# Kernel optimization log

Hardware: AMD Instinct MI355X
Metric: run time of the kernel (lower is better)

Reference implementation:

```python
import jax, jax.numpy as jnp
import numpy as np

B = 4096
N_QUBITS = 4
N_LAYERS = 3
C64 = jnp.complex64


def setup_inputs() -> dict:
    key = jax.random.key(0)
    ks = jax.random.split(key, 14)
    f = jax.random.normal
    return {
        "x": f(ks[0], (B, 1, 28, 28), jnp.float32),
        "qparams": f(ks[1], (N_LAYERS, N_QUBITS, 3), jnp.float32),
        "dw4_w": f(ks[2], (4, 1, 4, 4), jnp.float32) * 0.1,
        "dw4_b": f(ks[3], (4,), jnp.float32) * 0.1,
        "pw4_w": f(ks[4], (4, 4, 1, 1), jnp.float32) * 0.3,
        "pw4_b": f(ks[5], (4,), jnp.float32) * 0.1,
        "dw8_w": f(ks[6], (4, 1, 8, 8), jnp.float32) * 0.05,
        "dw8_b": f(ks[7], (4,), jnp.float32) * 0.1,
        "pw8_w": f(ks[8], (4, 4, 1, 1), jnp.float32) * 0.3,
        "pw8_b": f(ks[9], (4,), jnp.float32) * 0.1,
        "res_w": f(ks[10], (4, 1, 1, 1), jnp.float32) * 0.3,
        "res_b": f(ks[11], (4,), jnp.float32) * 0.1,
        "head_w": f(ks[12], (10, 4 * 3 * 14 * 14), jnp.float32) * 0.02,
        "head_b": f(ks[13], (10,), jnp.float32) * 0.02,
    }


def _rx(t):
    c = jnp.cos(t / 2).astype(C64)
    s = (-1j * jnp.sin(t / 2)).astype(C64)
    return jnp.stack([jnp.stack([c, s]), jnp.stack([s, c])])


def _ry(t):
    c = jnp.cos(t / 2)
    s = jnp.sin(t / 2)
    return jnp.stack([jnp.stack([c, -s]), jnp.stack([s, c])]).astype(C64)


def _rz(t):
    z = jnp.zeros((), C64)
    return jnp.stack([jnp.stack([jnp.exp(-0.5j * t).astype(C64), z]),
                      jnp.stack([z, jnp.exp(0.5j * t).astype(C64)])])


def _apply_1q(state, U, wire):
    # state: (n,2,2,2,2); U: (2,2) shared across patches
    st = jnp.moveaxis(state, wire + 1, -1)
    st = jnp.einsum('ij,n...j->n...i', U, st)
    return jnp.moveaxis(st, -1, wire + 1)


def _apply_1q_batched(state, U, wire):
    # U: (n,2,2), one gate per patch (input encoding)
    st = jnp.moveaxis(state, wire + 1, -1)
    st = jnp.einsum('nij,n...j->n...i', U, st)
    return jnp.moveaxis(st, -1, wire + 1)


def _cnot(state, c, t):
    a, b = jnp.split(state, 2, axis=c + 1)
    return jnp.concatenate([a, jnp.flip(b, axis=t + 1)], axis=c + 1)


def _quantum_features(patches, params):
    # patches: (n,4) angles; returns (n,4) PauliZ expectations
    n = patches.shape[0]
    state = jnp.zeros((n, 16), C64).at[:, 0].set(1.0).reshape(n, 2, 2, 2, 2)
    c = jnp.cos(patches / 2)
    s = jnp.sin(patches / 2)
    for q in range(N_QUBITS):
        Uq = jnp.stack([jnp.stack([c[:, q], -s[:, q]], -1),
                        jnp.stack([s[:, q], c[:, q]], -1)], -2).astype(C64)
        state = _apply_1q_batched(state, Uq, q)
    for l in range(N_LAYERS):
        for q in range(N_QUBITS):
            state = _apply_1q(state, _rx(params[l, q, 0]), q)
            state = _apply_1q(state, _ry(params[l, q, 1]), q)
            state = _apply_1q(state, _rz(params[l, q, 2]), q)
        for q in range(N_QUBITS - 1):
            state = _cnot(state, q, q + 1)
        state = _cnot(state, N_QUBITS - 1, 0)
    probs = jnp.real(state * jnp.conj(state))  # (n,2,2,2,2)
    ez = [jnp.sum(jnp.take(probs, 0, axis=q + 1) - jnp.take(probs, 1, axis=q + 1),
                  axis=(1, 2, 3)) for q in range(N_QUBITS)]
    return jnp.stack(ez, -1).astype(jnp.float32)


def _conv(x, w, b, stride):
    y = jax.lax.conv_general_dilated(x, w, (stride, stride), 'VALID',
                                     dimension_numbers=('NCHW', 'OIHW', 'NCHW'))
    return y + b[None, :, None, None]


def _forward(x, qparams, dw4_w, dw4_b, pw4_w, pw4_b, dw8_w, dw8_b, pw8_w, pw8_b,
             res_w, res_b, head_w, head_b):
    b = x.shape[0]
    # residual branch: 1x1 conv then 2x2 avg-pool down to the 14x14 grid
    res = _conv(x, res_w, res_b, 1)                      # (B,4,28,28)
    res = res.reshape(b, 4, 14, 2, 14, 2).mean(axis=(3, 5))  # (B,4,14,14)
    # quantum branch over non-overlapping 2x2 patches
    patches = x[:, 0].reshape(b, 14, 2, 14, 2).transpose(0, 1, 3, 2, 4)
    patches = patches.reshape(b * 14 * 14, 4)
    feat2 = _quantum_features(patches, qparams).reshape(b, 14, 14, 4)
    # multi-scale conv branches, upsampled (nearest) to the 14x14 grid
    feat4 = jax.nn.relu(_conv(_conv(x, dw4_w, dw4_b, 4), pw4_w, pw4_b, 1))  # (B,4,7,7)
    feat4 = jnp.repeat(jnp.repeat(feat4, 2, axis=2), 2, axis=3)             # (B,4,14,14)
    feat8 = jax.nn.relu(_conv(_conv(x, dw8_w, dw8_b, 8), pw8_w, pw8_b, 1))  # (B,4,3,3)
    feat8 = jax.image.resize(feat8, (b, 4, 14, 14), 'nearest')
    f4 = jnp.transpose(feat4, (0, 2, 3, 1))
    f8 = jnp.transpose(feat8, (0, 2, 3, 1))
    r = jnp.transpose(res, (0, 2, 3, 1))
    out = jnp.concatenate([feat2, f4, f8], axis=3) + jnp.tile(r, (1, 1, 1, 3))
    logits = out.reshape(b, -1) @ head_w.T + head_b
    return jax.nn.log_softmax(logits, axis=-1)


def reference(x, qparams, dw4_w, dw4_b, pw4_w, pw4_b, dw8_w, dw8_b, pw8_w, pw8_b,
              res_w, res_b, head_w, head_b):
    return _forward(x, qparams, dw4_w, dw4_b, pw4_w, pw4_b, dw8_w, dw8_b,
                    pw8_w, pw8_b, res_w, res_b, head_w, head_b)
```

## Files before the change

### kernel.cpp

```cpp
#include <hip/hip_runtime.h>

#define WS_T    0
#define WS_HQ   512
#define WS_WA   8352
#define WS_H4   10312
#define WS_H8   12272
#define WS_C10  12632

__device__ __forceinline__ float4 f4fma(const float4 a, const float s, const float4 c) {
  return {fmaf(a.x, s, c.x), fmaf(a.y, s, c.y), fmaf(a.z, s, c.z), fmaf(a.w, s, c.w)};
}
__device__ __forceinline__ float4 f4fma4(const float4 a, const float4 b, const float4 c) {
  return {fmaf(a.x, b.x, c.x), fmaf(a.y, b.y, c.y), fmaf(a.z, b.z, c.z), fmaf(a.w, b.w, c.w)};
}
__device__ __forceinline__ float hsum4(const float4 a) {
  return a.x + a.y + a.z + a.w;
}

__global__ __launch_bounds__(256) void prep_kernel(
    const float* __restrict__ qp, const float* __restrict__ hw,
    const float* __restrict__ res_w, const float* __restrict__ res_b,
    const float* __restrict__ hb, float* __restrict__ ws) {
  __shared__ float row[2352];
  __shared__ float cred[4];
  __shared__ float Sr[16][16];
  __shared__ float Si[16][16];
  __shared__ float csc[36], css[36];
  __shared__ float Afs[256][4];
  const int t = threadIdx.x;

  if (blockIdx.x < 10) {
    const int k = blockIdx.x;
    for (int i = t; i < 2352; i += 256) row[i] = hw[k * 2352 + i];
    __syncthreads();
    float cpart = 0.f;
    if (t < 196) {
      const int b12 = t * 12;
      float4 h = {row[b12], row[b12 + 1], row[b12 + 2], row[b12 + 3]};
      ((float4*)(ws + WS_HQ))[k * 196 + t] = h;
      float wa = 0.f;
#pragma unroll
      for (int c = 0; c < 4; ++c) {
        const float s3 = row[b12 + c] + row[b12 + 4 + c] + row[b12 + 8 + c];
        wa += res_w[c] * s3;
        cpart += res_b[c] * s3;
      }
      ws[WS_WA + k * 196 + t] = wa;
    }
    if (t < 49) {
      const int i4 = t / 7, j4 = t % 7;
      float4 s = {0.f, 0.f, 0.f, 0.f};
#pragma unroll
      for (int di = 0; di < 2; ++di)
#pragma unroll
        for (int dj = 0; dj < 2; ++dj) {
          const int pos = (2 * i4 + di) * 14 + 2 * j4 + dj;
          s.x += row[pos * 12 + 4]; s.y += row[pos * 12 + 5];
          s.z += row[pos * 12 + 6]; s.w += row[pos * 12 + 7];
        }
      ((float4*)(ws + WS_H4))[k * 49 + t] = s;
    }
    if (t < 9) {
      const int i8 = t / 3, j8 = t % 3;
      const int pi0 = (i8 == 0) ? 0 : ((i8 == 1) ? 5 : 9);
      const int pi1 = (i8 == 0) ? 5 : ((i8 == 1) ? 9 : 14);
      const int pj0 = (j8 == 0) ? 0 : ((j8 == 1) ? 5 : 9);
      const int pj1 = (j8 == 0) ? 5 : ((j8 == 1) ? 9 : 14);
      float4 s = {0.f, 0.f, 0.f, 0.f};
      for (int pi = pi0; pi < pi1; ++pi)
        for (int pj = pj0; pj < pj1; ++pj) {
          const int pos = pi * 14 + pj;
          s.x += row[pos * 12 + 8]; s.y += row[pos * 12 + 9];
          s.z += row[pos * 12 + 10]; s.w += row[pos * 12 + 11];
        }
      ((float4*)(ws + WS_H8))[k * 9 + t] = s;
    }
#pragma unroll
    for (int off = 32; off > 0; off >>= 1) cpart += __shfl_xor(cpart, off);
    if ((t & 63) == 0) cred[t >> 6] = cpart;
    __syncthreads();
    if (t == 0) ws[WS_C10 + k] = hb[k] + cred[0] + cred[1] + cred[2] + cred[3];
    return;
  }

  if (t < 36) {
    float th = 0.5f * qp[t];
    csc[t] = cosf(th);
    css[t] = sinf(th);
  }
  Sr[t >> 4][t & 15] = ((t >> 4) == (t & 15)) ? 1.f : 0.f;
  Si[t >> 4][t & 15] = 0.f;
  __syncthreads();

  const int col = t >> 3, pp = t & 7;
  for (int l = 0; l < 3; ++l) {
    for (int q = 0; q < 4; ++q) {
      const int m = 8 >> q;
      for (int r = 0; r < 3; ++r) {
        if (t < 128) {
          const float c = csc[l * 12 + q * 3 + r];
          const float s = css[l * 12 + q * 3 + r];
          const int k = ((pp & ~(m - 1)) << 1) | (pp & (m - 1));
          const int k1 = k | m;
          float a0r = Sr[col][k],  a0i = Si[col][k];
          float a1r = Sr[col][k1], a1i = Si[col][k1];
          float n0r, n0i, n1r, n1i;
          if (r == 0) {
            n0r = c * a0r + s * a1i;  n0i = c * a0i - s * a1r;
            n1r = c * a1r + s * a0i;  n1i = c * a1i - s * a0r;
          } else if (r == 1) {
            n0r = c * a0r - s * a1r;  n0i = c * a0i - s * a1i;
            n1r = s * a0r + c * a1r;  n1i = s * a0i + c * a1i;
          } else {
            n0r = c * a0r + s * a0i;  n0i = c * a0i - s * a0r;
            n1r = c * a1r - s * a1i;  n1i = c * a1i + s * a1r;
          }
          Sr[col][k] = n0r;  Si[col][k] = n0i;
          Sr[col][k1] = n1r; Si[col][k1] = n1i;
        }
        __syncthreads();
      }
    }
    for (int e = 0; e < 4; ++e) {
      if (t < 64) {
        const int c2 = t >> 2, p2 = t & 3;
        const int mc = 8 >> e;
        const int mt = 8 >> ((e + 1) & 3);
        const int rest = 15 & ~(mc | mt);
        const int rl = rest & (-rest);
        const int rh = rest ^ rl;
        const int k = mc | ((p2 & 1) ? rl : 0) | ((p2 & 2) ? rh : 0);
        const int k1 = k | mt;
        float tr = Sr[c2][k]; Sr[c2][k] = Sr[c2][k1]; Sr[c2][k1] = tr;
        float ti = Si[c2][k]; Si[c2][k] = Si[c2][k1]; Si[c2][k1] = ti;
      }
      __syncthreads();
    }
  }

  {
    const int i = t >> 4, j = t & 15;
    float a0 = 0.f, a1 = 0.f, a2 = 0.f, a3 = 0.f;
    for (int k = 0; k < 16; ++k) {
      float pr = Sr[i][k] * Sr[j][k] + Si[i][k] * Si[j][k];
      a0 += (k & 8) ? -pr : pr;
      a1 += (k & 4) ? -pr : pr;
      a2 += (k & 2) ? -pr : pr;
      a3 += (k & 1) ? -pr : pr;
    }
    Afs[t][0] = a0; Afs[t][1] = a1; Afs[t][2] = a2; Afs[t][3] = a3;
  }
  __syncthreads();

  for (int o = t; o < 324; o += 256) {
    const int mi = o >> 2, q = o & 3;
    const int m0 = mi / 27, m1 = (mi / 9) % 3, m2 = (mi / 3) % 3, m3 = mi % 3;
    const int mm[4] = {m0, m1, m2, m3};
    float acc = 0.f;
    for (int c = 0; c < 16; ++c) {
      int ii = 0, jj = 0; float sg = 1.f;
      for (int qb = 0; qb < 4; ++qb) {
        const int cb = (c >> qb) & 1, bit = 8 >> qb, mq = mm[qb];
        if (mq == 2) { if (cb) ii |= bit; else jj |= bit; }
        else if (cb) { ii |= bit; jj |= bit; if (mq == 1) sg = -sg; }
      }
      acc += sg * Afs[ii * 16 + jj][q];
    }
    ws[WS_T + mi * 4 + q] = acc * 0.0625f;
  }
}

__global__ __launch_bounds__(256, 4) void qmain_kernel(
    const float* __restrict__ x, const float4* __restrict__ T4,
    const float4* __restrict__ HQ4, const float* __restrict__ WA,
    const float4* __restrict__ H44, const float4* __restrict__ H84,
    const float* __restrict__ C10,
    const float* __restrict__ dw4_w, const float* __restrict__ dw4_b,
    const float* __restrict__ pw4_w, const float* __restrict__ pw4_b,
    const float* __restrict__ dw8_w, const float* __restrict__ dw8_b,
    const float* __restrict__ pw8_w, const float* __restrict__ pw8_b,
    float* __restrict__ out, const int B) {
  __shared__ __align__(16) float xs[4 * 792];
  const int t = threadIdx.x;
  const int w = t >> 6, lane = t & 63;
  const int img = blockIdx.x * 4 + w;
  float* xw = xs + w * 792;
  const float4* xw4 = (const float4*)xw;

  if (img < B) {
    const float4* xg = (const float4*)(x + img * 784);
#pragma unroll
    for (int it = 0; it < 4; ++it) {
      const int idx = it * 64 + lane;
      if (idx < 196) ((float4*)xw)[idx] = xg[idx];
    }
  }
  __syncthreads();

  if (img >= B) return;

  float acc[10];
#pragma unroll
  for (int k = 0; k < 10; ++k) acc[k] = 0.f;

#pragma unroll 1
  for (int r = 0; r < 4; ++r) {
    const int p = r * 64 + lane;
    if (p < 196) {
      const int pi = p / 14, pj = p % 14;
      const int base = 56 * pi + 2 * pj;
      const float2 a01 = *(const float2*)(xw + base);
      const float2 a23 = *(const float2*)(xw + base + 28);
      const float a0 = a01.x, a1 = a01.y, a2 = a23.x, a3 = a23.y;
      float c0, s0, c1, s1, c2, s2, c3, s3;
      __sincosf(a0, &s0, &c0);
      __sincosf(a1, &s1, &c1);
      __sincosf(a2, &s2, &c2);
      __sincosf(a3, &s3, &c3);
      const float w01[9] = {1.f, c1, s1, c0, c0 * c1, c0 * s1, s0, s0 * c1, s0 * s1};
      float4 e = {0.f, 0.f, 0.f, 0.f};
#pragma unroll
      for (int g = 0; g < 9; ++g) {
        const float4 t0 = T4[g * 9 + 0], t1 = T4[g * 9 + 1], t2 = T4[g * 9 + 2];
        const float4 t3 = T4[g * 9 + 3], t4 = T4[g * 9 + 4], t5 = T4[g * 9 + 5];
        const float4 t6 = T4[g * 9 + 6], t7 = T4[g * 9 + 7], t8 = T4[g * 9 + 8];
        const float4 u0 = f4fma(t2, s3, f4fma(t1, c3, t0));
        const float4 u1 = f4fma(t5, s3, f4fma(t4, c3, t3));
        const float4 u2 = f4fma(t8, s3, f4fma(t7, c3, t6));
        const float4 inner = f4fma(u2, s2, f4fma(u1, c2, u0));
        e = f4fma(inner, w01[g], e);
      }
      const float avg = 0.25f * (a0 + a1 + a2 + a3);
#pragma unroll
      for (int k = 0; k < 10; ++k) {
        const float4 h = HQ4[k * 196 + p];
        acc[k] += fmaf(h.x, e.x, fmaf(h.y, e.y,
                  fmaf(h.z, e.z, fmaf(h.w, e.w, WA[k * 196 + p] * avg))));
      }
    } else {
      const int u = p - 196;
      if (u < 49) {
        const int i = u / 7, j = u % 7;
        const float4* w44 = (const float4*)dw4_w;
        float4 q0 = {0.f, 0.f, 0.f, 0.f}, q1 = q0, q2 = q0, q3 = q0;
#pragma unroll
        for (int uu = 0; uu < 4; ++uu) {
          const float4 xa = xw4[(4 * i + uu) * 7 + j];
          q0 = f4fma4(w44[0 + uu], xa, q0);
          q1 = f4fma4(w44[4 + uu], xa, q1);
          q2 = f4fma4(w44[8 + uu], xa, q2);
          q3 = f4fma4(w44[12 + uu], xa, q3);
        }
        const float y0 = hsum4(q0) + dw4_b[0];
        const float y1 = hsum4(q1) + dw4_b[1];
        const float y2 = hsum4(q2) + dw4_b[2];
        const float y3 = hsum4(q3) + dw4_b[3];
        float z[4];
#pragma unroll
        for (int o = 0; o < 4; ++o) {
          float zz = pw4_b[o];
          zz = fmaf(pw4_w[o * 4 + 0], y0, zz);
          zz = fmaf(pw4_w[o * 4 + 1], y1, zz);
          zz = fmaf(pw4_w[o * 4 + 2], y2, zz);
          zz = fmaf(pw4_w[o * 4 + 3], y3, zz);
          z[o] = fmaxf(zz, 0.f);
        }
#pragma unroll
        for (int k = 0; k < 10; ++k) {
          const float4 h = H44[k * 49 + u];
          acc[k] += fmaf(h.x, z[0], fmaf(h.y, z[1], fmaf(h.z, z[2], h.w * z[3])));
        }
      } else if (u < 58) {
        const int pos = u - 49;
        const int i8 = pos / 3, j8 = pos % 3;
        const float4* w84 = (const float4*)dw8_w;
        float4 e0 = {0.f, 0.f, 0.f, 0.f}, e1 = e0, e2 = e0, e3 = e0;
#pragma unroll
        for (int uu = 0; uu < 8; ++uu) {
          const float4 xa = xw4[(8 * i8 + uu) * 7 + 2 * j8];
          const float4 xb = xw4[(8 * i8 + uu) * 7 + 2 * j8 + 1];
          e0 = f4fma4(w84[0 + uu * 2], xa, e0);
          e0 = f4fma4(w84[1 + uu * 2], xb, e0);
          e1 = f4fma4(w84[16 + uu * 2], xa, e1);
          e1 = f4fma4(w84[17 + uu * 2], xb, e1);
          e2 = f4fma4(w84[32 + uu * 2], xa, e2);
          e2 = f4fma4(w84[33 + uu * 2], xb, e2);
          e3 = f4fma4(w84[48 + uu * 2], xa, e3);
          e3 = f4fma4(w84[49 + uu * 2], xb, e3);
        }
        const float d0 = hsum4(e0) + dw8_b[0];
        const float d1 = hsum4(e1) + dw8_b[1];
        const float d2 = hsum4(e2) + dw8_b[2];
        const float d3 = hsum4(e3) + dw8_b[3];
        float z[4];
#pragma unroll
        for (int o = 0; o < 4; ++o) {
          float zz = pw8_b[o];
          zz = fmaf(pw8_w[o * 4 + 0], d0, zz);
          zz = fmaf(pw8_w[o * 4 + 1], d1, zz);
          zz = fmaf(pw8_w[o * 4 + 2], d2, zz);
          zz = fmaf(pw8_w[o * 4 + 3], d3, zz);
          z[o] = fmaxf(zz, 0.f);
        }
#pragma unroll
        for (int k = 0; k < 10; ++k) {
          const float4 h = H84[k * 9 + pos];
          acc[k] += fmaf(h.x, z[0], fmaf(h.y, z[1], fmaf(h.z, z[2], h.w * z[3])));
        }
      }
    }
  }

#pragma unroll
  for (int k = 0; k < 10; ++k) {
    float v = acc[k];
    v += __shfl_xor(v, 1);
    v += __shfl_xor(v, 2);
    v += __shfl_xor(v, 4);
    v += __shfl_xor(v, 8);
    v += __shfl_xor(v, 16);
    v += __shfl_xor(v, 32);
    acc[k] = v;
  }

  float lg[10], m = -1e30f;
#pragma unroll
  for (int k = 0; k < 10; ++k) {
    lg[k] = acc[k] + C10[k];
    m = fmaxf(m, lg[k]);
  }
  float se = 0.f;
#pragma unroll
  for (int k = 0; k < 10; ++k) se += __expf(lg[k] - m);
  const float ls = m + __logf(se);
  if (lane < 10) {
    float v = lg[0];
#pragma unroll
    for (int k = 1; k < 10; ++k)
      if (lane == k) v = lg[k];
    out[img * 10 + lane] = v - ls;
  }
}

extern "C" void kernel_launch(void* const* d_in, const int* in_sizes, int n_in,
                              void* d_out, int out_size, void* d_ws, size_t ws_size,
                              hipStream_t stream) {
  const float* x      = (const float*)d_in[0];
  const float* qp     = (const float*)d_in[1];
  const float* dw4_w  = (const float*)d_in[2];
  const float* dw4_b  = (const float*)d_in[3];
  const float* pw4_w  = (const float*)d_in[4];
  const float* pw4_b  = (const float*)d_in[5];
  const float* dw8_w  = (const float*)d_in[6];
  const float* dw8_b  = (const float*)d_in[7];
  const float* pw8_w  = (const float*)d_in[8];
  const float* pw8_b  = (const float*)d_in[9];
  const float* res_w  = (const float*)d_in[10];
  const float* res_b  = (const float*)d_in[11];
  const float* head_w = (const float*)d_in[12];
  const float* head_b = (const float*)d_in[13];
  float* out = (float*)d_out;
  float* ws = (float*)d_ws;
  const int B = in_sizes[0] / 784;

  hipLaunchKernelGGL(prep_kernel, dim3(11), dim3(256), 0, stream,
                     qp, head_w, res_w, res_b, head_b, ws);
  hipLaunchKernelGGL(qmain_kernel, dim3((B + 3) / 4), dim3(256), 0, stream,
                     x, (const float4*)(ws + WS_T),
                     (const float4*)(ws + WS_HQ), ws + WS_WA,
                     (const float4*)(ws + WS_H4), (const float4*)(ws + WS_H8),
                     ws + WS_C10,
                     dw4_w, dw4_b, pw4_w, pw4_b, dw8_w, dw8_b, pw8_w, pw8_b,
                     out, B);
}
```

Before: 33.86 us.

## Split each image across two wavefronts and run prep quantum sim in one wave

The main kernel now assigns two wavefronts per image instead of one. Each wave processes half of the 196 quantum patches, one wave handles the 4x4 conv branch and the other the 8x8 branch, and the partial logits are combined through shared memory before log-softmax. The launch grid doubles and the occupancy hint is raised to 8. The prep kernel's state simulation now runs in a single 64-thread wavefront, which removes the many block-wide barriers. The cost is an extra LDS reduction and barrier in the main kernel, plus more blocks to schedule.

After: 76.70 us. 127% more time.

```diff
diff --git a/kernel.cpp b/kernel.cpp
--- a/kernel.cpp
+++ b/kernel.cpp
@@ -83,23 +83,30 @@
     return;
   }
 
+  if (t >= 64) return;
+
   if (t < 36) {
     float th = 0.5f * qp[t];
     csc[t] = cosf(th);
     css[t] = sinf(th);
   }
-  Sr[t >> 4][t & 15] = ((t >> 4) == (t & 15)) ? 1.f : 0.f;
-  Si[t >> 4][t & 15] = 0.f;
-  __syncthreads();
-
-  const int col = t >> 3, pp = t & 7;
+#pragma unroll
+  for (int h = 0; h < 4; ++h) {
+    const int idx = t + 64 * h;
+    Sr[idx >> 4][idx & 15] = ((idx >> 4) == (idx & 15)) ? 1.f : 0.f;
+    Si[idx >> 4][idx & 15] = 0.f;
+  }
+
   for (int l = 0; l < 3; ++l) {
     for (int q = 0; q < 4; ++q) {
       const int m = 8 >> q;
       for (int r = 0; r < 3; ++r) {
-        if (t < 128) {
-          const float c = csc[l * 12 + q * 3 + r];
-          const float s = css[l * 12 + q * 3 + r];
+        const float c = csc[l * 12 + q * 3 + r];
+        const float s = css[l * 12 + q * 3 + r];
+#pragma unroll
+        for (int h = 0; h < 2; ++h) {
+          const int idx = t + 64 * h;
+          const int col = idx >> 3, pp = idx & 7;
           const int k = ((pp & ~(m - 1)) << 1) | (pp & (m - 1));
           const int k1 = k | m;
           float a0r = Sr[col][k],  a0i = Si[col][k];
@@ -118,28 +125,26 @@
           Sr[col][k] = n0r;  Si[col][k] = n0i;
           Sr[col][k1] = n1r; Si[col][k1] = n1i;
         }
-        __syncthreads();
       }
     }
     for (int e = 0; e < 4; ++e) {
-      if (t < 64) {
-        const int c2 = t >> 2, p2 = t & 3;
-        const int mc = 8 >> e;
-        const int mt = 8 >> ((e + 1) & 3);
-        const int rest = 15 & ~(mc | mt);
-        const int rl = rest & (-rest);
-        const int rh = rest ^ rl;
-        const int k = mc | ((p2 & 1) ? rl : 0) | ((p2 & 2) ? rh : 0);
-        const int k1 = k | mt;
-        float tr = Sr[c2][k]; Sr[c2][k] = Sr[c2][k1]; Sr[c2][k1] = tr;
-        float ti = Si[c2][k]; Si[c2][k] = Si[c2][k1]; Si[c2][k1] = ti;
-      }
-      __syncthreads();
-    }
-  }
-
-  {
-    const int i = t >> 4, j = t & 15;
+      const int c2 = t >> 2, p2 = t & 3;
+      const int mc = 8 >> e;
+      const int mt = 8 >> ((e + 1) & 3);
+      const int rest = 15 & ~(mc | mt);
+      const int rl = rest & (-rest);
+      const int rh = rest ^ rl;
+      const int k = mc | ((p2 & 1) ? rl : 0) | ((p2 & 2) ? rh : 0);
+      const int k1 = k | mt;
+      float tr = Sr[c2][k]; Sr[c2][k] = Sr[c2][k1]; Sr[c2][k1] = tr;
+      float ti = Si[c2][k]; Si[c2][k] = Si[c2][k1]; Si[c2][k1] = ti;
+    }
+  }
+
+#pragma unroll
+  for (int h = 0; h < 4; ++h) {
+    const int o = t + 64 * h;
+    const int i = o >> 4, j = o & 15;
     float a0 = 0.f, a1 = 0.f, a2 = 0.f, a3 = 0.f;
     for (int k = 0; k < 16; ++k) {
       float pr = Sr[i][k] * Sr[j][k] + Si[i][k] * Si[j][k];
@@ -148,29 +153,32 @@
       a2 += (k & 2) ? -pr : pr;
       a3 += (k & 1) ? -pr : pr;
     }
-    Afs[t][0] = a0; Afs[t][1] = a1; Afs[t][2] = a2; Afs[t][3] = a3;
-  }
-  __syncthreads();
-
-  for (int o = t; o < 324; o += 256) {
-    const int mi = o >> 2, q = o & 3;
-    const int m0 = mi / 27, m1 = (mi / 9) % 3, m2 = (mi / 3) % 3, m3 = mi % 3;
-    const int mm[4] = {m0, m1, m2, m3};
-    float acc = 0.f;
-    for (int c = 0; c < 16; ++c) {
-      int ii = 0, jj = 0; float sg = 1.f;
-      for (int qb = 0; qb < 4; ++qb) {
-        const int cb = (c >> qb) & 1, bit = 8 >> qb, mq = mm[qb];
-        if (mq == 2) { if (cb) ii |= bit; else jj |= bit; }
-        else if (cb) { ii |= bit; jj |= bit; if (mq == 1) sg = -sg; }
-      }
-      acc += sg * Afs[ii * 16 + jj][q];
-    }
-    ws[WS_T + mi * 4 + q] = acc * 0.0625f;
-  }
-}
-
-__global__ __launch_bounds__(256, 4) void qmain_kernel(
+    Afs[o][0] = a0; Afs[o][1] = a1; Afs[o][2] = a2; Afs[o][3] = a3;
+  }
+
+#pragma unroll
+  for (int h = 0; h < 6; ++h) {
+    const int o = t + 64 * h;
+    if (o < 324) {
+      const int mi = o >> 2, q = o & 3;
+      const int m0 = mi / 27, m1 = (mi / 9) % 3, m2 = (mi / 3) % 3, m3 = mi % 3;
+      const int mm[4] = {m0, m1, m2, m3};
+      float acc = 0.f;
+      for (int c = 0; c < 16; ++c) {
+        int ii = 0, jj = 0; float sg = 1.f;
+        for (int qb = 0; qb < 4; ++qb) {
+          const int cb = (c >> qb) & 1, bit = 8 >> qb, mq = mm[qb];
+          if (mq == 2) { if (cb) ii |= bit; else jj |= bit; }
+          else if (cb) { ii |= bit; jj |= bit; if (mq == 1) sg = -sg; }
+        }
+        acc += sg * Afs[ii * 16 + jj][q];
+      }
+      ws[WS_T + mi * 4 + q] = acc * 0.0625f;
+    }
+  }
+}
+
+__global__ __launch_bounds__(256, 8) void qmain_kernel(
     const float* __restrict__ x, const float4* __restrict__ T4,
     const float4* __restrict__ HQ4, const float* __restrict__ WA,
     const float4* __restrict__ H44, const float4* __restrict__ H84,
@@ -180,66 +188,74 @@
     const float* __restrict__ dw8_w, const float* __restrict__ dw8_b,
     const float* __restrict__ pw8_w, const float* __restrict__ pw8_b,
     float* __restrict__ out, const int B) {
-  __shared__ __align__(16) float xs[4 * 792];
+  __shared__ __align__(16) float xs[2 * 792];
+  __shared__ float accw[4][10];
   const int t = threadIdx.x;
   const int w = t >> 6, lane = t & 63;
-  const int img = blockIdx.x * 4 + w;
-  float* xw = xs + w * 792;
+  const int il = w >> 1, pw = w & 1;
+  const int img = blockIdx.x * 2 + il;
+  float* xw = xs + il * 792;
   const float4* xw4 = (const float4*)xw;
-
-  if (img < B) {
+  const bool ok = (img < B);
+
+  if (ok) {
     const float4* xg = (const float4*)(x + img * 784);
-#pragma unroll
-    for (int it = 0; it < 4; ++it) {
-      const int idx = it * 64 + lane;
-      if (idx < 196) ((float4*)xw)[idx] = xg[idx];
+    const int i0 = pw * 98 + lane;
+    ((float4*)xw)[i0] = xg[i0];
+    if (lane < 34) {
+      const int i1 = pw * 98 + 64 + lane;
+      ((float4*)xw)[i1] = xg[i1];
+    }
+  }
+
+  float acc[10];
+#pragma unroll
+  for (int k = 0; k < 10; ++k) acc[k] = 0.f;
+
+  if (ok) {
+#pragma unroll 1
+    for (int r = 0; r < 2; ++r) {
+      const int p = pw * 98 + r * 64 + lane;
+      if (r == 0 || lane < 34) {
+        const int pi = p / 14, pj = p % 14;
+        const int base = 56 * pi + 2 * pj;
+        const float2 a01 = *(const float2*)(xw + base);
+        const float2 a23 = *(const float2*)(xw + base + 28);
+        const float a0 = a01.x, a1 = a01.y, a2 = a23.x, a3 = a23.y;
+        float c0, s0, c1, s1, c2, s2, c3, s3;
+        __sincosf(a0, &s0, &c0);
+        __sincosf(a1, &s1, &c1);
+        __sincosf(a2, &s2, &c2);
+        __sincosf(a3, &s3, &c3);
+        const float w01[9] = {1.f, c1, s1, c0, c0 * c1, c0 * s1, s0, s0 * c1, s0 * s1};
+        float4 e = {0.f, 0.f, 0.f, 0.f};
+#pragma unroll
+        for (int g = 0; g < 9; ++g) {
+          const float4 t0 = T4[g * 9 + 0], t1 = T4[g * 9 + 1], t2 = T4[g * 9 + 2];
+          const float4 t3 = T4[g * 9 + 3], t4 = T4[g * 9 + 4], t5 = T4[g * 9 + 5];
+          const float4 t6 = T4[g * 9 + 6], t7 = T4[g * 9 + 7], t8 = T4[g * 9 + 8];
+          const float4 u0 = f4fma(t2, s3, f4fma(t1, c3, t0));
+          const float4 u1 = f4fma(t5, s3, f4fma(t4, c3, t3));
+          const float4 u2 = f4fma(t8, s3, f4fma(t7, c3, t6));
+          const float4 inner = f4fma(u2, s2, f4fma(u1, c2, u0));
+          e = f4fma(inner, w01[g], e);
+        }
+        const float avg = 0.25f * (a0 + a1 + a2 + a3);
+#pragma unroll
+        for (int k = 0; k < 10; ++k) {
+          const float4 h = HQ4[k * 196 + p];
+          acc[k] += fmaf(h.x, e.x, fmaf(h.y, e.y,
+                    fmaf(h.z, e.z, fmaf(h.w, e.w, WA[k * 196 + p] * avg))));
+        }
+      }
     }
   }
   __syncthreads();
 
-  if (img >= B) return;
-
-  float acc[10];
-#pragma unroll
-  for (int k = 0; k < 10; ++k) acc[k] = 0.f;
-
-#pragma unroll 1
-  for (int r = 0; r < 4; ++r) {
-    const int p = r * 64 + lane;
-    if (p < 196) {
-      const int pi = p / 14, pj = p % 14;
-      const int base = 56 * pi + 2 * pj;
-      const float2 a01 = *(const float2*)(xw + base);
-      const float2 a23 = *(const float2*)(xw + base + 28);
-      const float a0 = a01.x, a1 = a01.y, a2 = a23.x, a3 = a23.y;
-      float c0, s0, c1, s1, c2, s2, c3, s3;
-      __sincosf(a0, &s0, &c0);
-      __sincosf(a1, &s1, &c1);
-      __sincosf(a2, &s2, &c2);
-      __sincosf(a3, &s3, &c3);
-      const float w01[9] = {1.f, c1, s1, c0, c0 * c1, c0 * s1, s0, s0 * c1, s0 * s1};
-      float4 e = {0.f, 0.f, 0.f, 0.f};
-#pragma unroll
-      for (int g = 0; g < 9; ++g) {
-        const float4 t0 = T4[g * 9 + 0], t1 = T4[g * 9 + 1], t2 = T4[g * 9 + 2];
-        const float4 t3 = T4[g * 9 + 3], t4 = T4[g * 9 + 4], t5 = T4[g * 9 + 5];
-        const float4 t6 = T4[g * 9 + 6], t7 = T4[g * 9 + 7], t8 = T4[g * 9 + 8];
-        const float4 u0 = f4fma(t2, s3, f4fma(t1, c3, t0));
-        const float4 u1 = f4fma(t5, s3, f4fma(t4, c3, t3));
-        const float4 u2 = f4fma(t8, s3, f4fma(t7, c3, t6));
-        const float4 inner = f4fma(u2, s2, f4fma(u1, c2, u0));
-        e = f4fma(inner, w01[g], e);
-      }
-      const float avg = 0.25f * (a0 + a1 + a2 + a3);
-#pragma unroll
-      for (int k = 0; k < 10; ++k) {
-        const float4 h = HQ4[k * 196 + p];
-        acc[k] += fmaf(h.x, e.x, fmaf(h.y, e.y,
-                  fmaf(h.z, e.z, fmaf(h.w, e.w, WA[k * 196 + p] * avg))));
-      }
-    } else {
-      const int u = p - 196;
-      if (u < 49) {
+  if (ok) {
+    if (pw == 0) {
+      if (lane < 49) {
+        const int u = lane;
         const int i = u / 7, j = u % 7;
         const float4* w44 = (const float4*)dw4_w;
         float4 q0 = {0.f, 0.f, 0.f, 0.f}, q1 = q0, q2 = q0, q3 = q0;
@@ -270,8 +286,10 @@
           const float4 h = H44[k * 49 + u];
           acc[k] += fmaf(h.x, z[0], fmaf(h.y, z[1], fmaf(h.z, z[2], h.w * z[3])));
         }
-      } else if (u < 58) {
-        const int pos = u - 49;
+      }
+    } else {
+      if (lane < 9) {
+        const int pos = lane;
         const int i8 = pos / 3, j8 = pos % 3;
         const float4* w84 = (const float4*)dw8_w;
         float4 e0 = {0.f, 0.f, 0.f, 0.f}, e1 = e0, e2 = e0, e3 = e0;
@@ -322,23 +340,29 @@
     v += __shfl_xor(v, 32);
     acc[k] = v;
   }
-
-  float lg[10], m = -1e30f;
-#pragma unroll
-  for (int k = 0; k < 10; ++k) {
-    lg[k] = acc[k] + C10[k];
-    m = fmaxf(m, lg[k]);
-  }
-  float se = 0.f;
-#pragma unroll
-  for (int k = 0; k < 10; ++k) se += __expf(lg[k] - m);
-  const float ls = m + __logf(se);
-  if (lane < 10) {
-    float v = lg[0];
+  {
+    float v = acc[0];
 #pragma unroll
     for (int k = 1; k < 10; ++k)
-      if (lane == k) v = lg[k];
-    out[img * 10 + lane] = v - ls;
+      if (lane == k) v = acc[k];
+    if (lane < 10) accw[w][lane] = v;
+  }
+  __syncthreads();
+
+  if (pw == 0 && ok) {
+    float lg = -1e30f;
+    if (lane < 10) lg = accw[w][lane] + accw[w + 1][lane] + C10[lane];
+    float mx = lg;
+    mx = fmaxf(mx, __shfl_xor(mx, 1));
+    mx = fmaxf(mx, __shfl_xor(mx, 2));
+    mx = fmaxf(mx, __shfl_xor(mx, 4));
+    mx = fmaxf(mx, __shfl_xor(mx, 8));
+    float ex = (lane < 10) ? __expf(lg - mx) : 0.f;
+    ex += __shfl_xor(ex, 1);
+    ex += __shfl_xor(ex, 2);
+    ex += __shfl_xor(ex, 4);
+    ex += __shfl_xor(ex, 8);
+    if (lane < 10) out[img * 10 + lane] = lg - mx - __logf(ex);
   }
 }
 
@@ -365,7 +389,7 @@
 
   hipLaunchKernelGGL(prep_kernel, dim3(11), dim3(256), 0, stream,
                      qp, head_w, res_w, res_b, head_b, ws);
-  hipLaunchKernelGGL(qmain_kernel, dim3((B + 3) / 4), dim3(256), 0, stream,
+  hipLaunchKernelGGL(qmain_kernel, dim3((B + 1) / 2), dim3(256), 0, stream,
                      x, (const float4*)(ws + WS_T),
                      (const float4*)(ws + WS_HQ), ws + WS_WA,
                      (const float4*)(ws + WS_H4), (const float4*)(ws + WS_H8),
```

## Remove block barriers and give each lane four quantum patches

Applied to the files above, without the earlier changes.

The prep kernel now runs its state-vector simulation on a single 64-lane wavefront and drops every __syncthreads. It relies on in-order shared-memory access within one wavefront instead of block barriers. The main kernel drops the post-load block barrier, since each wavefront only reads the image slice it loaded itself. It also remaps work so lanes 0-48 each handle four quantum patches plus one 4x4 conv output, and lanes 49-57 handle the 8x8 conv, which shares each T4 coefficient load across four patches and removes the divergent four-pass loop. The catch is that correctness now depends on implicit wave-synchronous behaviour, and lanes 58-63 sit idle.

Result: no change. 33.89 us (+0.1%).

```diff
diff --git a/kernel.cpp b/kernel.cpp
--- a/kernel.cpp
+++ b/kernel.cpp
@@ -83,23 +83,30 @@
     return;
   }
 
+  if (t >= 64) return;
+
   if (t < 36) {
     float th = 0.5f * qp[t];
     csc[t] = cosf(th);
     css[t] = sinf(th);
   }
-  Sr[t >> 4][t & 15] = ((t >> 4) == (t & 15)) ? 1.f : 0.f;
-  Si[t >> 4][t & 15] = 0.f;
-  __syncthreads();
-
-  const int col = t >> 3, pp = t & 7;
+#pragma unroll
+  for (int h = 0; h < 4; ++h) {
+    const int idx = t + 64 * h;
+    Sr[idx >> 4][idx & 15] = ((idx >> 4) == (idx & 15)) ? 1.f : 0.f;
+    Si[idx >> 4][idx & 15] = 0.f;
+  }
+
   for (int l = 0; l < 3; ++l) {
     for (int q = 0; q < 4; ++q) {
       const int m = 8 >> q;
       for (int r = 0; r < 3; ++r) {
-        if (t < 128) {
-          const float c = csc[l * 12 + q * 3 + r];
-          const float s = css[l * 12 + q * 3 + r];
+        const float c = csc[l * 12 + q * 3 + r];
+        const float s = css[l * 12 + q * 3 + r];
+#pragma unroll
+        for (int h = 0; h < 2; ++h) {
+          const int idx = t + 64 * h;
+          const int col = idx >> 3, pp = idx & 7;
           const int k = ((pp & ~(m - 1)) << 1) | (pp & (m - 1));
           const int k1 = k | m;
           float a0r = Sr[col][k],  a0i = Si[col][k];
@@ -118,28 +125,26 @@
           Sr[col][k] = n0r;  Si[col][k] = n0i;
           Sr[col][k1] = n1r; Si[col][k1] = n1i;
         }
-        __syncthreads();
       }
     }
     for (int e = 0; e < 4; ++e) {
-      if (t < 64) {
-        const int c2 = t >> 2, p2 = t & 3;
-        const int mc = 8 >> e;
-        const int mt = 8 >> ((e + 1) & 3);
-        const int rest = 15 & ~(mc | mt);
-        const int rl = rest & (-rest);
-        const int rh = rest ^ rl;
-        const int k = mc | ((p2 & 1) ? rl : 0) | ((p2 & 2) ? rh : 0);
-        const int k1 = k | mt;
-        float tr = Sr[c2][k]; Sr[c2][k] = Sr[c2][k1]; Sr[c2][k1] = tr;
-        float ti = Si[c2][k]; Si[c2][k] = Si[c2][k1]; Si[c2][k1] = ti;
-      }
-      __syncthreads();
-    }
-  }
-
-  {
-    const int i = t >> 4, j = t & 15;
+      const int c2 = t >> 2, p2 = t & 3;
+      const int mc = 8 >> e;
+      const int mt = 8 >> ((e + 1) & 3);
+      const int rest = 15 & ~(mc | mt);
+      const int rl = rest & (-rest);
+      const int rh = rest ^ rl;
+      const int k = mc | ((p2 & 1) ? rl : 0) | ((p2 & 2) ? rh : 0);
+      const int k1 = k | mt;
+      float tr = Sr[c2][k]; Sr[c2][k] = Sr[c2][k1]; Sr[c2][k1] = tr;
+      float ti = Si[c2][k]; Si[c2][k] = Si[c2][k1]; Si[c2][k1] = ti;
+    }
+  }
+
+#pragma unroll
+  for (int h = 0; h < 4; ++h) {
+    const int o = t + 64 * h;
+    const int i = o >> 4, j = o & 15;
     float a0 = 0.f, a1 = 0.f, a2 = 0.f, a3 = 0.f;
     for (int k = 0; k < 16; ++k) {
       float pr = Sr[i][k] * Sr[j][k] + Si[i][k] * Si[j][k];
@@ -148,25 +153,28 @@
       a2 += (k & 2) ? -pr : pr;
       a3 += (k & 1) ? -pr : pr;
     }
-    Afs[t][0] = a0; Afs[t][1] = a1; Afs[t][2] = a2; Afs[t][3] = a3;
-  }
-  __syncthreads();
-
-  for (int o = t; o < 324; o += 256) {
-    const int mi = o >> 2, q = o & 3;
-    const int m0 = mi / 27, m1 = (mi / 9) % 3, m2 = (mi / 3) % 3, m3 = mi % 3;
-    const int mm[4] = {m0, m1, m2, m3};
-    float acc = 0.f;
-    for (int c = 0; c < 16; ++c) {
-      int ii = 0, jj = 0; float sg = 1.f;
-      for (int qb = 0; qb < 4; ++qb) {
-        const int cb = (c >> qb) & 1, bit = 8 >> qb, mq = mm[qb];
-        if (mq == 2) { if (cb) ii |= bit; else jj |= bit; }
-        else if (cb) { ii |= bit; jj |= bit; if (mq == 1) sg = -sg; }
-      }
-      acc += sg * Afs[ii * 16 + jj][q];
-    }
-    ws[WS_T + mi * 4 + q] = acc * 0.0625f;
+    Afs[o][0] = a0; Afs[o][1] = a1; Afs[o][2] = a2; Afs[o][3] = a3;
+  }
+
+#pragma unroll
+  for (int h = 0; h < 6; ++h) {
+    const int o = t + 64 * h;
+    if (o < 324) {
+      const int mi = o >> 2, q = o & 3;
+      const int m0 = mi / 27, m1 = (mi / 9) % 3, m2 = (mi / 3) % 3, m3 = mi % 3;
+      const int mm[4] = {m0, m1, m2, m3};
+      float acc = 0.f;
+      for (int c = 0; c < 16; ++c) {
+        int ii = 0, jj = 0; float sg = 1.f;
+        for (int qb = 0; qb < 4; ++qb) {
+          const int cb = (c >> qb) & 1, bit = 8 >> qb, mq = mm[qb];
+          if (mq == 2) { if (cb) ii |= bit; else jj |= bit; }
+          else if (cb) { ii |= bit; jj |= bit; if (mq == 1) sg = -sg; }
+        }
+        acc += sg * Afs[ii * 16 + jj][q];
+      }
+      ws[WS_T + mi * 4 + q] = acc * 0.0625f;
+    }
   }
 }
 
@@ -186,8 +194,9 @@
   const int img = blockIdx.x * 4 + w;
   float* xw = xs + w * 792;
   const float4* xw4 = (const float4*)xw;
-
-  if (img < B) {
+  const bool ok = (img < B);
+
+  if (ok) {
     const float4* xg = (const float4*)(x + img * 784);
 #pragma unroll
     for (int it = 0; it < 4; ++it) {
@@ -195,121 +204,132 @@
       if (idx < 196) ((float4*)xw)[idx] = xg[idx];
     }
   }
-  __syncthreads();
-
-  if (img >= B) return;
 
   float acc[10];
 #pragma unroll
   for (int k = 0; k < 10; ++k) acc[k] = 0.f;
 
-#pragma unroll 1
-  for (int r = 0; r < 4; ++r) {
-    const int p = r * 64 + lane;
-    if (p < 196) {
-      const int pi = p / 14, pj = p % 14;
-      const int base = 56 * pi + 2 * pj;
+  if (ok && lane < 49) {
+    float cc[4][4], ss[4][4], av[4];
+#pragma unroll
+    for (int s = 0; s < 4; ++s) {
+      const int p = 49 * s + lane;
+      const int base = 56 * (p / 14) + 2 * (p % 14);
       const float2 a01 = *(const float2*)(xw + base);
       const float2 a23 = *(const float2*)(xw + base + 28);
-      const float a0 = a01.x, a1 = a01.y, a2 = a23.x, a3 = a23.y;
-      float c0, s0, c1, s1, c2, s2, c3, s3;
-      __sincosf(a0, &s0, &c0);
-      __sincosf(a1, &s1, &c1);
-      __sincosf(a2, &s2, &c2);
-      __sincosf(a3, &s3, &c3);
-      const float w01[9] = {1.f, c1, s1, c0, c0 * c1, c0 * s1, s0, s0 * c1, s0 * s1};
-      float4 e = {0.f, 0.f, 0.f, 0.f};
-#pragma unroll
-      for (int g = 0; g < 9; ++g) {
-        const float4 t0 = T4[g * 9 + 0], t1 = T4[g * 9 + 1], t2 = T4[g * 9 + 2];
-        const float4 t3 = T4[g * 9 + 3], t4 = T4[g * 9 + 4], t5 = T4[g * 9 + 5];
-        const float4 t6 = T4[g * 9 + 6], t7 = T4[g * 9 + 7], t8 = T4[g * 9 + 8];
+      __sincosf(a01.x, &ss[s][0], &cc[s][0]);
+      __sincosf(a01.y, &ss[s][1], &cc[s][1]);
+      __sincosf(a23.x, &ss[s][2], &cc[s][2]);
+      __sincosf(a23.y, &ss[s][3], &cc[s][3]);
+      av[s] = 0.25f * (a01.x + a01.y + a23.x + a23.y);
+    }
+    float4 e[4];
+#pragma unroll
+    for (int s = 0; s < 4; ++s) e[s] = {0.f, 0.f, 0.f, 0.f};
+#pragma unroll 1
+    for (int g = 0; g < 9; ++g) {
+      const float4 t0 = T4[g * 9 + 0], t1 = T4[g * 9 + 1], t2 = T4[g * 9 + 2];
+      const float4 t3 = T4[g * 9 + 3], t4 = T4[g * 9 + 4], t5 = T4[g * 9 + 5];
+      const float4 t6 = T4[g * 9 + 6], t7 = T4[g * 9 + 7], t8 = T4[g * 9 + 8];
+      const int m0 = g / 3, m1 = g % 3;
+#pragma unroll
+      for (int s = 0; s < 4; ++s) {
+        const float c3 = cc[s][3], s3 = ss[s][3];
         const float4 u0 = f4fma(t2, s3, f4fma(t1, c3, t0));
         const float4 u1 = f4fma(t5, s3, f4fma(t4, c3, t3));
         const float4 u2 = f4fma(t8, s3, f4fma(t7, c3, t6));
-        const float4 inner = f4fma(u2, s2, f4fma(u1, c2, u0));
-        e = f4fma(inner, w01[g], e);
-      }
-      const float avg = 0.25f * (a0 + a1 + a2 + a3);
+        const float4 inner = f4fma(u2, ss[s][2], f4fma(u1, cc[s][2], u0));
+        const float f0 = (m0 == 0) ? 1.f : ((m0 == 1) ? cc[s][0] : ss[s][0]);
+        const float f1 = (m1 == 0) ? 1.f : ((m1 == 1) ? cc[s][1] : ss[s][1]);
+        const float wf = (m0 == 0) ? f1 : ((m1 == 0) ? f0 : f0 * f1);
+        e[s] = f4fma(inner, wf, e[s]);
+      }
+    }
+#pragma unroll
+    for (int k = 0; k < 10; ++k) {
+      float a = 0.f;
+#pragma unroll
+      for (int s = 0; s < 4; ++s) {
+        const int p = 49 * s + lane;
+        const float4 h = HQ4[k * 196 + p];
+        a += fmaf(h.x, e[s].x, fmaf(h.y, e[s].y,
+             fmaf(h.z, e[s].z, fmaf(h.w, e[s].w, WA[k * 196 + p] * av[s]))));
+      }
+      acc[k] = a;
+    }
+    {
+      const int u = lane;
+      const int i = u / 7, j = u % 7;
+      const float4* w44 = (const float4*)dw4_w;
+      float4 q0 = {0.f, 0.f, 0.f, 0.f}, q1 = q0, q2 = q0, q3 = q0;
+#pragma unroll
+      for (int uu = 0; uu < 4; ++uu) {
+        const float4 xa = xw4[(4 * i + uu) * 7 + j];
+        q0 = f4fma4(w44[0 + uu], xa, q0);
+        q1 = f4fma4(w44[4 + uu], xa, q1);
+        q2 = f4fma4(w44[8 + uu], xa, q2);
+        q3 = f4fma4(w44[12 + uu], xa, q3);
+      }
+      const float y0 = hsum4(q0) + dw4_b[0];
+      const float y1 = hsum4(q1) + dw4_b[1];
+      const float y2 = hsum4(q2) + dw4_b[2];
+      const float y3 = hsum4(q3) + dw4_b[3];
+      float z[4];
+#pragma unroll
+      for (int o = 0; o < 4; ++o) {
+        float zz = pw4_b[o];
+        zz = fmaf(pw4_w[o * 4 + 0], y0, zz);
+        zz = fmaf(pw4_w[o * 4 + 1], y1, zz);
+        zz = fmaf(pw4_w[o * 4 + 2], y2, zz);
+        zz = fmaf(pw4_w[o * 4 + 3], y3, zz);
+        z[o] = fmaxf(zz, 0.f);
+      }
 #pragma unroll
       for (int k = 0; k < 10; ++k) {
-        const float4 h = HQ4[k * 196 + p];
-        acc[k] += fmaf(h.x, e.x, fmaf(h.y, e.y,
-                  fmaf(h.z, e.z, fmaf(h.w, e.w, WA[k * 196 + p] * avg))));
-      }
-    } else {
-      const int u = p - 196;
-      if (u < 49) {
-        const int i = u / 7, j = u % 7;
-        const float4* w44 = (const float4*)dw4_w;
-        float4 q0 = {0.f, 0.f, 0.f, 0.f}, q1 = q0, q2 = q0, q3 = q0;
-#pragma unroll
-        for (int uu = 0; uu < 4; ++uu) {
-          const float4 xa = xw4[(4 * i + uu) * 7 + j];
-          q0 = f4fma4(w44[0 + uu], xa, q0);
-          q1 = f4fma4(w44[4 + uu], xa, q1);
-          q2 = f4fma4(w44[8 + uu], xa, q2);
-          q3 = f4fma4(w44[12 + uu], xa, q3);
-        }
-        const float y0 = hsum4(q0) + dw4_b[0];
-        const float y1 = hsum4(q1) + dw4_b[1];
-        const float y2 = hsum4(q2) + dw4_b[2];
-        const float y3 = hsum4(q3) + dw4_b[3];
-        float z[4];
-#pragma unroll
-        for (int o = 0; o < 4; ++o) {
-          float zz = pw4_b[o];
-          zz = fmaf(pw4_w[o * 4 + 0], y0, zz);
-          zz = fmaf(pw4_w[o * 4 + 1], y1, zz);
-          zz = fmaf(pw4_w[o * 4 + 2], y2, zz);
-          zz = fmaf(pw4_w[o * 4 + 3], y3, zz);
-          z[o] = fmaxf(zz, 0.f);
-        }
-#pragma unroll
-        for (int k = 0; k < 10; ++k) {
-          const float4 h = H44[k * 49 + u];
-          acc[k] += fmaf(h.x, z[0], fmaf(h.y, z[1], fmaf(h.z, z[2], h.w * z[3])));
-        }
-      } else if (u < 58) {
-        const int pos = u - 49;
-        const int i8 = pos / 3, j8 = pos % 3;
-        const float4* w84 = (const float4*)dw8_w;
-        float4 e0 = {0.f, 0.f, 0.f, 0.f}, e1 = e0, e2 = e0, e3 = e0;
-#pragma unroll
-        for (int uu = 0; uu < 8; ++uu) {
-          const float4 xa = xw4[(8 * i8 + uu) * 7 + 2 * j8];
-          const float4 xb = xw4[(8 * i8 + uu) * 7 + 2 * j8 + 1];
-          e0 = f4fma4(w84[0 + uu * 2], xa, e0);
-          e0 = f4fma4(w84[1 + uu * 2], xb, e0);
-          e1 = f4fma4(w84[16 + uu * 2], xa, e1);
-          e1 = f4fma4(w84[17 + uu * 2], xb, e1);
-          e2 = f4fma4(w84[32 + uu * 2], xa, e2);
-          e2 = f4fma4(w84[33 + uu * 2], xb, e2);
-          e3 = f4fma4(w84[48 + uu * 2], xa, e3);
-          e3 = f4fma4(w84[49 + uu * 2], xb, e3);
-        }
-        const float d0 = hsum4(e0) + dw8_b[0];
-        const float d1 = hsum4(e1) + dw8_b[1];
-        const float d2 = hsum4(e2) + dw8_b[2];
-        const float d3 = hsum4(e3) + dw8_b[3];
-        float z[4];
-#pragma unroll
-        for (int o = 0; o < 4; ++o) {
-          float zz = pw8_b[o];
-          zz = fmaf(pw8_w[o * 4 + 0], d0, zz);
-          zz = fmaf(pw8_w[o * 4 + 1], d1, zz);
-          zz = fmaf(pw8_w[o * 4 + 2], d2, zz);
-          zz = fmaf(pw8_w[o * 4 + 3], d3, zz);
-          z[o] = fmaxf(zz, 0.f);
-        }
-#pragma unroll
-        for (int k = 0; k < 10; ++k) {
-          const float4 h = H84[k * 9 + pos];
-          acc[k] += fmaf(h.x, z[0], fmaf(h.y, z[1], fmaf(h.z, z[2], h.w * z[3])));
-        }
-      }
-    }
-  }
+        const float4 h = H44[k * 49 + u];
+        acc[k] += fmaf(h.x, z[0], fmaf(h.y, z[1], fmaf(h.z, z[2], h.w * z[3])));
+      }
+    }
+  } else if (ok && lane >= 49 && lane < 58) {
+    const int pos = lane - 49;
+    const int i8 = pos / 3, j8 = pos % 3;
+    const float4* w84 = (const float4*)dw8_w;
+    float4 e0 = {0.f, 0.f, 0.f, 0.f}, e1 = e0, e2 = e0, e3 = e0;
+#pragma unroll
+    for (int uu = 0; uu < 8; ++uu) {
+      const float4 xa = xw4[(8 * i8 + uu) * 7 + 2 * j8];
+      const float4 xb = xw4[(8 * i8 + uu) * 7 + 2 * j8 + 1];
+      e0 = f4fma4(w84[0 + uu * 2], xa, e0);
+      e0 = f4fma4(w84[1 + uu * 2], xb, e0);
+      e1 = f4fma4(w84[16 + uu * 2], xa, e1);
+      e1 = f4fma4(w84[17 + uu * 2], xb, e1);
+      e2 = f4fma4(w84[32 + uu * 2], xa, e2);
+      e2 = f4fma4(w84[33 + uu * 2], xb, e2);
+      e3 = f4fma4(w84[48 + uu * 2], xa, e3);
+      e3 = f4fma4(w84[49 + uu * 2], xb, e3);
+    }
+    const float d0 = hsum4(e0) + dw8_b[0];
+    const float d1 = hsum4(e1) + dw8_b[1];
+    const float d2 = hsum4(e2) + dw8_b[2];
+    const float d3 = hsum4(e3) + dw8_b[3];
+    float z[4];
+#pragma unroll
+    for (int o = 0; o < 4; ++o) {
+      float zz = pw8_b[o];
+      zz = fmaf(pw8_w[o * 4 + 0], d0, zz);
+      zz = fmaf(pw8_w[o * 4 + 1], d1, zz);
+      zz = fmaf(pw8_w[o * 4 + 2], d2, zz);
+      zz = fmaf(pw8_w[o * 4 + 3], d3, zz);
+      z[o] = fmaxf(zz, 0.f);
+    }
+#pragma unroll
+    for (int k = 0; k < 10; ++k) {
+      const float4 h = H84[k * 9 + pos];
+      acc[k] += fmaf(h.x, z[0], fmaf(h.y, z[1], fmaf(h.z, z[2], h.w * z[3])));
+    }
+  }
+
+  if (!ok) return;
 
 #pragma unroll
   for (int k = 0; k < 10; ++k) {
```
